# Optimization experiments

Measured on AMD Instinct MI355X. Metric: run time of the kernel, lower is better.

The kernel has to match this reference:

```python
import jax, jax.numpy as jnp
import numpy as np

N, B, S, A = 4, 32768, 512, 64
H = 256          # hidden_size
NH = 16          # effective number of heads = attend_dim (range(attend_dim) bug in source)
D = 16           # attend_dim = hidden // attend_heads
EPS_BN = 1e-5


def setup_inputs() -> dict:
    key = jax.random.key(0)
    ks = jax.random.split(key, 16)
    sc = 0.05
    return {
        "states": jax.random.normal(ks[0], (N, B, S), dtype=jnp.float32),
        "actions": jax.random.normal(ks[1], (N, B, A), dtype=jnp.float32),
        # per-agent state+action encoder (enc_fc1)
        "Wenc": jax.random.normal(ks[2], (N, S + A, H), dtype=jnp.float32) * sc,
        "benc": jax.random.normal(ks[3], (N, H), dtype=jnp.float32) * sc,
        # per-agent state encoder (s_enc_fc1)
        "Ws": jax.random.normal(ks[4], (N, S, H), dtype=jnp.float32) * sc,
        "bs": jax.random.normal(ks[5], (N, H), dtype=jnp.float32) * sc,
        # shared per-head extractors (no bias on key/selector; bias on value)
        "Wk": jax.random.normal(ks[6], (NH, H, D), dtype=jnp.float32) * sc,
        "Wsel": jax.random.normal(ks[7], (NH, H, D), dtype=jnp.float32) * sc,
        "Wv": jax.random.normal(ks[8], (NH, H, D), dtype=jnp.float32) * sc,
        "bv": jax.random.normal(ks[9], (NH, D), dtype=jnp.float32) * sc,
        # per-agent critic MLP (input = H + NH*D = 2H)
        "Wc1": jax.random.normal(ks[10], (N, 2 * H, H), dtype=jnp.float32) * sc,
        "bc1": jax.random.normal(ks[11], (N, H), dtype=jnp.float32) * sc,
        "Wc2": jax.random.normal(ks[12], (N, H, A), dtype=jnp.float32) * sc,
        "bc2": jax.random.normal(ks[13], (N, A), dtype=jnp.float32) * sc,
    }


def _lrelu(x):
    return jax.nn.leaky_relu(x, 0.01)


def _bn(x):
    # BatchNorm1d(affine=False), training mode: biased batch stats over batch axis
    m = x.mean(axis=1, keepdims=True)
    v = x.var(axis=1, keepdims=True)
    return (x - m) * jax.lax.rsqrt(v + EPS_BN)


def reference(states, actions, Wenc, benc, Ws, bs, Wk, Wsel, Wv, bv, Wc1, bc1, Wc2, bc2):
    n, b = states.shape[0], states.shape[1]
    # state+action encodings per agent: [n, B, H]
    sa = jnp.concatenate([states, actions], axis=-1)
    sa_enc = _lrelu(jnp.einsum('nbi,nih->nbh', _bn(sa), Wenc) + benc[:, None, :])
    # state encodings per agent: [n, B, H]
    s_enc = _lrelu(jnp.einsum('nbs,nsh->nbh', _bn(states), Ws) + bs[:, None, :])
    # per-head keys/values/selectors: [NH, n, B, D]
    keys = jnp.einsum('nbh,ehd->enbd', sa_enc, Wk)
    vals = _lrelu(jnp.einsum('nbh,ehd->enbd', sa_enc, Wv) + bv[:, None, None, :])
    sel = jnp.einsum('nbh,ehd->enbd', s_enc, Wsel)
    # attention of agent i over agents j != i (self excluded via -inf mask)
    logits = jnp.einsum('eibd,ejbd->eibj', sel, keys) / jnp.sqrt(jnp.float32(D))
    self_mask = jnp.eye(n, dtype=bool)[None, :, None, :]  # [1, i, 1, j]
    probs = jax.nn.softmax(jnp.where(self_mask, -1e9, logits), axis=-1)
    # weighted values: [n, B, NH, D] (head-major concat order)
    other = jnp.einsum('eibj,ejbd->ibed', probs, vals)
    critic_in = jnp.concatenate([s_enc, other.reshape(n, b, NH * D)], axis=-1)  # [n, B, 2H]
    h = _lrelu(jnp.einsum('nbc,nch->nbh', critic_in, Wc1) + bc1[:, None, :])
    all_q = jnp.einsum('nbh,nha->nba', h, Wc2) + bc2[:, None, :]  # [n, B, A]
    idx = jnp.argmax(actions, axis=-1)  # [n, B]
    q = jnp.take_along_axis(all_q, idx[..., None], axis=-1)  # [n, B, 1]
    return q
```

## Files before the change

kernel.cpp:

```cpp
#include <hip/hip_runtime.h>
#include <hip/hip_bf16.h>
#include <cstdint>
#include <cstddef>

using bf16 = __hip_bfloat16;
typedef __attribute__((ext_vector_type(8))) short bf16x8v;
typedef __attribute__((ext_vector_type(4))) short bf16x4v;
typedef __attribute__((ext_vector_type(4))) float f32x4v;

constexpr int Nn = 4;
constexpr int Bb = 32768;
constexpr int Ss = 512;
constexpr int Av = 64;
constexpr int SA = 576;
constexpr float BN_EPS = 1e-5f;

__device__ __forceinline__ float lrelu(float v){ return v >= 0.f ? v : 0.01f * v; }
__device__ __forceinline__ float bf2f(bf16 x){ return __bfloat162float(x); }
__device__ __forceinline__ short f2bf(float v){
  union { bf16 b; short s; } u; u.b = __float2bfloat16(v); return u.s;
}

__device__ __forceinline__ void gload16(const void* g, void* l){
  __builtin_amdgcn_global_load_lds(
      (const __attribute__((address_space(1))) unsigned int*)g,
      (__attribute__((address_space(3))) unsigned int*)l, 16, 0, 0);
}

template<bool WRX>
__global__ __launch_bounds__(256) void conv_stats(const float* __restrict__ states,
                                                  const float* __restrict__ actions,
                                                  float* __restrict__ ssum,
                                                  float* __restrict__ ssq,
                                                  short* __restrict__ Xbf){
  const int n  = blockIdx.z;
  const int tx = threadIdx.x;
  const int ty = threadIdx.y;
  const int g  = blockIdx.x * 64 + tx;
  const bool on = g < (SA / 4);
  const int f  = g * 4;
  const float* p = nullptr; int step = 0;
  if (on){
    if (f < Ss){ p = states  + (size_t)n*Bb*Ss + f;        step = Ss; }
    else       { p = actions + (size_t)n*Bb*Av + (f - Ss); step = Av; }
  }
  float s0=0.f,s1=0.f,s2=0.f,s3=0.f,q0=0.f,q1=0.f,q2=0.f,q3=0.f;
  const int b0 = blockIdx.y * 512 + ty, bend = blockIdx.y * 512 + 512;
  if (on){
    for (int b = b0; b < bend; b += 4){
      float4 v = *(const float4*)(p + (size_t)b*step);
      if (WRX){
        short t4[4] __attribute__((aligned(8))) =
            { f2bf(v.x), f2bf(v.y), f2bf(v.z), f2bf(v.w) };
        *(bf16x4v*)&Xbf[((size_t)n*Bb + b)*SA + f] = *(bf16x4v*)t4;
      }
      s0 += v.x; q0 += v.x*v.x;
      s1 += v.y; q1 += v.y*v.y;
      s2 += v.z; q2 += v.z*v.z;
      s3 += v.w; q3 += v.w*v.w;
    }
  }
  __shared__ float rs[4][64][4], rq[4][64][4];
  rs[ty][tx][0]=s0; rs[ty][tx][1]=s1; rs[ty][tx][2]=s2; rs[ty][tx][3]=s3;
  rq[ty][tx][0]=q0; rq[ty][tx][1]=q1; rq[ty][tx][2]=q2; rq[ty][tx][3]=q3;
  __syncthreads();
  if (ty == 0 && on){
    #pragma unroll
    for (int j = 0; j < 4; j++){
      float ts = rs[0][tx][j]+rs[1][tx][j]+rs[2][tx][j]+rs[3][tx][j];
      float tq = rq[0][tx][j]+rq[1][tx][j]+rq[2][tx][j]+rq[3][tx][j];
      atomicAdd(&ssum[n*SA + f + j], ts);
      atomicAdd(&ssq [n*SA + f + j], tq);
    }
  }
}

__global__ void bn_finalize(const float* __restrict__ ssum, const float* __restrict__ ssq,
                            float* __restrict__ mean, float* __restrict__ rstd){
  int i = blockIdx.x * 256 + threadIdx.x;
  float m = ssum[i] * (1.f / Bb);
  float v = ssq[i] * (1.f / Bb) - m * m;
  v = fmaxf(v, 0.f);
  mean[i] = m;
  rstd[i] = rsqrtf(v + BN_EPS);
}

__global__ void bias_copy(const float* __restrict__ benc, const float* __restrict__ bsx,
                          float* __restrict__ besc){
  int i = blockIdx.x * 256 + threadIdx.x;
  if (i < Nn*512){
    int a = i >> 9, c = i & 511;
    besc[i] = (c < 256) ? benc[a*256 + c] : bsx[a*256 + (c - 256)];
  }
}

template<int HEAD>
__global__ __launch_bounds__(256) void foldT2(const float* __restrict__ src,
                                              const float* __restrict__ scale,
                                              const float* __restrict__ mean,
                                              float* __restrict__ bias_out,
                                              short* __restrict__ dst,
                                              int Ks, int Kd, int N,
                                              int aDst, int biasStride){
  const int a  = blockIdx.z;
  const int tx = threadIdx.x & 63;
  const int ty = threadIdx.x >> 6;
  const int f0 = blockIdx.x * 64 + ty * 16;
  const int c  = blockIdx.y * 64 + tx;
  const float* s = src + (HEAD ? 0 : (size_t)a*Ks*N);
  short tmp[16] __attribute__((aligned(16)));
  float bsum = 0.f;
  #pragma unroll
  for (int j = 0; j < 16; j++){
    const int f = f0 + j;
    float w = 0.f;
    if (f < Ks){
      w = HEAD ? s[(((size_t)(c >> 4))*Ks + f)*16 + (c & 15)]
               : s[(size_t)f*N + c];
      if (scale) w *= scale[a*SA + f];
      if (mean)  bsum += mean[a*SA + f] * w;
    }
    tmp[j] = f2bf(w);
  }
  short* d = dst + (size_t)a*aDst + (size_t)c*Kd + f0;
  *(bf16x8v*)d       = *(bf16x8v*)tmp;
  *(bf16x8v*)(d + 8) = *(bf16x8v*)(tmp + 8);
  if (mean){
    __shared__ float red[4][64];
    red[ty][tx] = bsum;
    __syncthreads();
    if (threadIdx.x < 64){
      float t = red[0][threadIdx.x] + red[1][threadIdx.x]
              + red[2][threadIdx.x] + red[3][threadIdx.x];
      atomicAdd(&bias_out[a*biasStride + blockIdx.y*64 + threadIdx.x], -t);
    }
  }
}

template<int BM,int BN,int WM,int WN,int K,int ASRC,int AP,bool ACT,bool OUTF32,int MODE>
__global__ __launch_bounds__(256) void mgemm2(const void* A1, const void* A2,
                                              const short* __restrict__ Wp, int wPerAgent,
                                              const float* __restrict__ bias, int biasStride,
                                              void* Out, int outPitch){
  __shared__ __align__(16) short As[BM*32];
  __shared__ __align__(16) short Bs[BN*32];
  const int tid  = threadIdx.x;
  const int a    = blockIdx.z;
  const int row0 = blockIdx.x * BM;
  const int col0 = blockIdx.y * BN;
  const short* Wb = Wp + (size_t)a * wPerAgent;
  constexpr int FM = BM/WM/16, FN = BN/WN/16;
  const int wid = tid >> 6, lane = tid & 63;
  const int wm = wid % WM, wn = wid / WM;
  const int rowB = wm*(BM/WM), colB = wn*(BN/WN);
  const int lrow = lane & 15, lq = lane >> 4;
  const int srow = lane >> 2;
  const int skc  = ((lane & 3) ^ ((srow >> 1) & 3)) * 8;
  const int rq   = lq ^ ((lrow >> 1) & 3);

  f32x4v acc[FM][FN];
  #pragma unroll
  for (int i = 0; i < FM; i++)
    #pragma unroll
    for (int j = 0; j < FN; j++) acc[i][j] = (f32x4v){0.f,0.f,0.f,0.f};

  constexpr int AB = BM/16;
  constexpr int BB = BN/16;

  for (int k0 = 0; k0 < K; k0 += 32){
    #pragma unroll
    for (int t = 0; t < AB/4; t++){
      const int bb = wid + t*4;
      const int r  = bb*16 + srow;
      const int f  = k0 + skc;
      const short* src;
      if constexpr (ASRC == 3)
        src = (f < 256) ? (const short*)A1 + ((size_t)a*Bb + row0 + r)*(size_t)AP + f
                        : (const short*)A2 + ((size_t)a*Bb + row0 + r)*256 + (f - 256);
      else
        src = (const short*)A1 + ((size_t)a*Bb + row0 + r)*(size_t)AP + f;
      gload16(src, &As[bb*512]);
    }
    #pragma unroll
    for (int t = 0; t < BB/4; t++){
      const int bb = wid + t*4;
      const int r  = bb*16 + srow;
      const short* src = Wb + (size_t)(col0 + r)*K + k0 + skc;
      gload16(src, &Bs[bb*512]);
    }
    __syncthreads();
    bf16x8v af[FM], bfr[FN];
    #pragma unroll
    for (int mi = 0; mi < FM; mi++)
      af[mi] = *(const bf16x8v*)&As[(rowB + mi*16 + lrow)*32 + rq*8];
    #pragma unroll
    for (int ni = 0; ni < FN; ni++)
      bfr[ni] = *(const bf16x8v*)&Bs[(colB + ni*16 + lrow)*32 + rq*8];
    #pragma unroll
    for (int mi = 0; mi < FM; mi++)
      #pragma unroll
      for (int ni = 0; ni < FN; ni++)
        acc[mi][ni] = __builtin_amdgcn_mfma_f32_16x16x32_bf16(af[mi], bfr[ni], acc[mi][ni], 0, 0, 0);
    __syncthreads();
  }
  #pragma unroll
  for (int mi = 0; mi < FM; mi++){
    const size_t gr = (size_t)a*Bb + row0 + rowB + mi*16 + lq*4;
    #pragma unroll
    for (int ni = 0; ni < FN; ni++){
      const int gc = col0 + colB + ni*16 + lrow;
      float bb; bool doact;
      if constexpr (MODE == 1){
        doact = (gc >= 256);
        bb = doact ? bias[gc - 256] : 0.f;
      } else {
        bb = bias ? bias[a*biasStride + gc] : 0.f;
        doact = ACT;
      }
      #pragma unroll
      for (int r = 0; r < 4; r++){
        float v = acc[mi][ni][r] + bb;
        if (doact) v = lrelu(v);
        if constexpr (OUTF32) ((float*)Out)[(gr + r)*(size_t)outPitch + gc] = v;
        else                  ((bf16*) Out)[(gr + r)*(size_t)outPitch + gc] = __float2bfloat16(v);
      }
    }
  }
}

union B8g { uint4 u; bf16 h[8]; };
__global__ __launch_bounds__(256) void attn_g(const bf16* __restrict__ KV,
                                              bf16* SO){
  const int t = blockIdx.x * 256 + threadIdx.x;
  const int e = t & 15;
  const size_t b = t >> 4;
  const size_t ofsKV = b*512 + e*16;
  const size_t ofsS  = b*256 + e*16;
  float S[4][16], Kf[4][16], Vf[4][16];
  #pragma unroll
  for (int i = 0; i < 4; i++){
    B8g u0, u1;
    const bf16* sp = SO + (size_t)i*Bb*256 + ofsS;
    u0.u = *(const uint4*)sp; u1.u = *(const uint4*)(sp + 8);
    #pragma unroll
    for (int l = 0; l < 8; l++){ S[i][l] = bf2f(u0.h[l]); S[i][8+l] = bf2f(u1.h[l]); }
    const bf16* kp = KV + (size_t)i*Bb*512 + ofsKV;
    u0.u = *(const uint4*)kp; u1.u = *(const uint4*)(kp + 8);
    #pragma unroll
    for (int l = 0; l < 8; l++){ Kf[i][l] = bf2f(u0.h[l]); Kf[i][8+l] = bf2f(u1.h[l]); }
    const bf16* vp = kp + 256;
    u0.u = *(const uint4*)vp; u1.u = *(const uint4*)(vp + 8);
    #pragma unroll
    for (int l = 0; l < 8; l++){ Vf[i][l] = bf2f(u0.h[l]); Vf[i][8+l] = bf2f(u1.h[l]); }
  }
  #pragma unroll
  for (int i = 0; i < 4; i++){
    float lg[4];
    #pragma unroll
    for (int j = 0; j < 4; j++){
      float d = 0.f;
      #pragma unroll
      for (int l = 0; l < 16; l++) d += S[i][l] * Kf[j][l];
      lg[j] = d * 0.25f;
    }
    lg[i] = -1e9f;
    float m = fmaxf(fmaxf(lg[0], lg[1]), fmaxf(lg[2], lg[3]));
    float p[4], s = 0.f;
    #pragma unroll
    for (int j = 0; j < 4; j++){ p[j] = expf(lg[j] - m); s += p[j]; }
    p[i] = 0.f;
    const float inv = 1.f / s;
    float o[16] = {};
    #pragma unroll
    for (int j = 0; j < 4; j++){
      const float pj = p[j] * inv;
      #pragma unroll
      for (int l = 0; l < 16; l++) o[l] += pj * Vf[j][l];
    }
    B8g w0, w1;
    #pragma unroll
    for (int l = 0; l < 8; l++){ w0.h[l] = __float2bfloat16(o[l]); w1.h[l] = __float2bfloat16(o[8+l]); }
    bf16* op = SO + (size_t)i*Bb*256 + ofsS;
    *(uint4*)op       = w0.u;
    *(uint4*)(op + 8) = w1.u;
  }
}

__global__ __launch_bounds__(256) void sel_q(const float* __restrict__ actions,
                                             const float* __restrict__ allq,
                                             float* __restrict__ out){
  const size_t i = (size_t)blockIdx.x * 256 + threadIdx.x;
  const float* ap = actions + i*64;
  float best = ap[0]; int bi = 0;
  for (int j = 1; j < 64; j++){
    float v = ap[j];
    if (v > best){ best = v; bi = j; }
  }
  out[i] = allq[i*64 + bi];
}

constexpr int RB = 4;

template<int K>
__device__ __forceinline__ void gemm4_glb(const float* __restrict__ st,
                                          const float* __restrict__ ac,
                                          const float* __restrict__ mean,
                                          const float* __restrict__ rstd,
                                          int a, int brow0, int tid,
                                          const float* __restrict__ W,
                                          const float* __restrict__ bias, bool act,
                                          float (*Xs)[68], float (*Wt)[264],
                                          float (*Sout)[256]){
  const int r = tid >> 6, c4 = (tid & 63) * 4;
  float acc[4] = {};
  for (int k0 = 0; k0 < K; k0 += 8){
    if (tid < 32){
      const int rb = tid >> 3, kq = tid & 7;
      const int f = k0 + kq;
      float v = (f < Ss) ? st[((size_t)a*Bb + brow0 + rb)*Ss + f]
                         : ac[((size_t)a*Bb + brow0 + rb)*Av + (f - Ss)];
      Xs[kq][rb] = (v - mean[a*SA + f]) * rstd[a*SA + f];
    }
    {
      const int wk = tid >> 5, wc = (tid & 31) * 8;
      const float* wp = W + (size_t)(k0 + wk) * 256 + wc;
      *(float4*)&Wt[wk][wc]     = *(const float4*)wp;
      *(float4*)&Wt[wk][wc + 4] = *(const float4*)(wp + 4);
    }
    __syncthreads();
    #pragma unroll
    for (int kk = 0; kk < 8; kk++){
      const float av = Xs[kk][r];
      float4 w = *(const float4*)&Wt[kk][c4];
      acc[0] += av*w.x; acc[1] += av*w.y; acc[2] += av*w.z; acc[3] += av*w.w;
    }
    __syncthreads();
  }
  float4 o;
  o.x = acc[0] + (bias ? bias[c4+0] : 0.f);
  o.y = acc[1] + (bias ? bias[c4+1] : 0.f);
  o.z = acc[2] + (bias ? bias[c4+2] : 0.f);
  o.w = acc[3] + (bias ? bias[c4+3] : 0.f);
  if (act){ o.x = lrelu(o.x); o.y = lrelu(o.y); o.z = lrelu(o.z); o.w = lrelu(o.w); }
  *(float4*)&Sout[a*RB + r][c4] = o;
}

template<int K, bool HEAD>
__device__ __forceinline__ void gemm4_lds(const float (*S1)[256], const float (*S2)[256],
                                          int a, int tid,
                                          const float* __restrict__ W,
                                          const float* __restrict__ bias, bool act,
                                          float (*Wt)[264], float (*Sout)[256]){
  const int r = tid >> 6, c4 = (tid & 63) * 4;
  float acc[4] = {};
  for (int k0 = 0; k0 < K; k0 += 8){
    if (HEAD){
      const int wk = tid >> 5, c8 = (tid & 31) * 8;
      const int e = c8 >> 4, d0 = c8 & 15;
      const float* wp = W + (size_t)e*(256*16) + (size_t)(k0 + wk)*16 + d0;
      *(float4*)&Wt[wk][c8]     = *(const float4*)wp;
      *(float4*)&Wt[wk][c8 + 4] = *(const float4*)(wp + 4);
    } else {
      const int wk = tid >> 5, wc = (tid & 31) * 8;
      const float* wp = W + (size_t)(k0 + wk)*256 + wc;
      *(float4*)&Wt[wk][wc]     = *(const float4*)wp;
      *(float4*)&Wt[wk][wc + 4] = *(const float4*)(wp + 4);
    }
    __syncthreads();
    const float (*src)[256] = (k0 < 256) ? S1 : S2;
    const int kb = (k0 < 256) ? k0 : k0 - 256;
    const float* arow = &src[a*RB + r][kb];
    #pragma unroll
    for (int kk = 0; kk < 8; kk++){
      const float av = arow[kk];
      float4 w = *(const float4*)&Wt[kk][c4];
      acc[0] += av*w.x; acc[1] += av*w.y; acc[2] += av*w.z; acc[3] += av*w.w;
    }
    __syncthreads();
  }
  float4 o;
  o.x = acc[0] + (bias ? bias[c4+0] : 0.f);
  o.y = acc[1] + (bias ? bias[c4+1] : 0.f);
  o.z = acc[2] + (bias ? bias[c4+2] : 0.f);
  o.w = acc[3] + (bias ? bias[c4+3] : 0.f);
  if (act){ o.x = lrelu(o.x); o.y = lrelu(o.y); o.z = lrelu(o.z); o.w = lrelu(o.w); }
  *(float4*)&Sout[a*RB + r][c4] = o;
}

__global__ __launch_bounds__(256) void fused(
    const float* __restrict__ states, const float* __restrict__ actions,
    const float* __restrict__ mean,  const float* __restrict__ rstd,
    const float* __restrict__ Wenc, const float* __restrict__ benc,
    const float* __restrict__ Wsx,  const float* __restrict__ bsx,
    const float* __restrict__ Wk,   const float* __restrict__ Wsel,
    const float* __restrict__ Wv,   const float* __restrict__ bv,
    const float* __restrict__ Wc1,  const float* __restrict__ bc1,
    const float* __restrict__ Wc2,  const float* __restrict__ bc2,
    float* __restrict__ qout){
  __shared__ float A [16][256];
  __shared__ float Bs2[16][256];
  __shared__ float C [16][256];
  __shared__ float Wt[8][264];
  __shared__ float Xs[8][68];
  __shared__ float Cq[4][68];
  const int tid   = threadIdx.x;
  const int brow0 = blockIdx.x * RB;
  for (int a = 0; a < Nn; a++)
    gemm4_glb<Ss>(states, actions, mean, rstd, a, brow0, tid,
                  Wsx + (size_t)a*Ss*256, bsx + a*256, true, Xs, Wt, A);
  __syncthreads();
  for (int a = 0; a < Nn; a++)
    gemm4_lds<256, true>(A, nullptr, a, tid, Wsel, nullptr, false, Wt, C);
  __syncthreads();
  for (int a = 0; a < Nn; a++)
    gemm4_glb<SA>(states, actions, mean, rstd, a, brow0, tid,
                  Wenc + (size_t)a*SA*256, benc + a*256, true, Xs, Wt, A);
  __syncthreads();
  for (int a = 0; a < Nn; a++)
    gemm4_lds<256, true>(A, nullptr, a, tid, Wk, nullptr, false, Wt, Bs2);
  __syncthreads();
  for (int a = 0; a < Nn; a++)
    gemm4_lds<256, true>(A, nullptr, a, tid, Wv, bv, true, Wt, A);
  __syncthreads();
  if (tid < 64){
    const int rb = tid >> 4, e = tid & 15;
    const int co = e * 16;
    float S[4][16], Kf[4][16], Vf[4][16];
    #pragma unroll
    for (int i = 0; i < 4; i++)
      #pragma unroll
      for (int l = 0; l < 16; l++){
        S[i][l]  = C  [i*RB + rb][co + l];
        Kf[i][l] = Bs2[i*RB + rb][co + l];
        Vf[i][l] = A  [i*RB + rb][co + l];
      }
    #pragma unroll
    for (int i = 0; i < 4; i++){
      float lg[4];
      #pragma unroll
      for (int j = 0; j < 4; j++){
        float d = 0.f;
        #pragma unroll
        for (int l = 0; l < 16; l++) d += S[i][l] * Kf[j][l];
        lg[j] = d * 0.25f;
      }
      lg[i] = -1e9f;
      float m = fmaxf(fmaxf(lg[0], lg[1]), fmaxf(lg[2], lg[3]));
      float p[4], s = 0.f;
      #pragma unroll
      for (int j = 0; j < 4; j++){ p[j] = expf(lg[j] - m); s += p[j]; }
      p[i] = 0.f;
      const float inv = 1.f / s;
      float o[16] = {};
      #pragma unroll
      for (int j = 0; j < 4; j++){
        const float pj = p[j] * inv;
        #pragma unroll
        for (int l = 0; l < 16; l++) o[l] += pj * Vf[j][l];
      }
      #pragma unroll
      for (int l = 0; l < 16; l++) C[i*RB + rb][co + l] = o[l];
    }
  }
  __syncthreads();
  for (int a = 0; a < Nn; a++)
    gemm4_glb<Ss>(states, actions, mean, rstd, a, brow0, tid,
                  Wsx + (size_t)a*Ss*256, bsx + a*256, true, Xs, Wt, A);
  __syncthreads();
  for (int a = 0; a < Nn; a++)
    gemm4_lds<512, false>(A, C, a, tid, Wc1 + (size_t)a*512*256, bc1 + a*256, true, Wt, Bs2);
  __syncthreads();
  for (int a = 0; a < Nn; a++){
    const int r2 = tid >> 6, c2 = tid & 63;
    float acc = 0.f;
    for (int k0 = 0; k0 < 256; k0 += 8){
      const int wk = tid >> 5, wc = (tid & 31) * 2;
      const float* wp = Wc2 + (size_t)a*256*64 + (size_t)(k0 + wk)*64 + wc;
      Wt[wk][wc]     = wp[0];
      Wt[wk][wc + 1] = wp[1];
      __syncthreads();
      #pragma unroll
      for (int kk = 0; kk < 8; kk++) acc += Bs2[a*RB + r2][k0 + kk] * Wt[kk][c2];
      __syncthreads();
    }
    Cq[r2][c2] = acc + bc2[a*64 + c2];
    __syncthreads();
    if (tid < RB){
      const float* ap = actions + ((size_t)a*Bb + brow0 + tid)*Av;
      float best = ap[0]; int bi = 0;
      for (int j = 1; j < Av; j++){
        float v = ap[j];
        if (v > best){ best = v; bi = j; }
      }
      qout[(size_t)a*Bb + brow0 + tid] = Cq[tid][bi];
    }
    __syncthreads();
  }
}

extern "C" void kernel_launch(void* const* d_in, const int* in_sizes, int n_in,
                              void* d_out, int out_size, void* d_ws, size_t ws_size,
                              hipStream_t stream){
  (void)in_sizes; (void)n_in; (void)out_size;
  const float* states  = (const float*)d_in[0];
  const float* actions = (const float*)d_in[1];
  const float* Wenc    = (const float*)d_in[2];
  const float* benc    = (const float*)d_in[3];
  const float* Wsx     = (const float*)d_in[4];
  const float* bsx     = (const float*)d_in[5];
  const float* Wk      = (const float*)d_in[6];
  const float* Wsel    = (const float*)d_in[7];
  const float* Wv      = (const float*)d_in[8];
  const float* bv      = (const float*)d_in[9];
  const float* Wc1     = (const float*)d_in[10];
  const float* bc1     = (const float*)d_in[11];
  const float* Wc2     = (const float*)d_in[12];
  const float* bc2     = (const float*)d_in[13];
  float* qout = (float*)d_out;

  char* base = (char*)d_ws;
  float* ssum = (float*)base;
  float* ssq  = ssum + Nn*SA;
  float* mean = ssq  + Nn*SA;
  float* rstd = mean + Nn*SA;
  size_t off = 4*Nn*SA*sizeof(float);
  float* besc  = (float*)(base + off); off += Nn*512*sizeof(float);
  short* Wes_p = (short*)(base + off); off += (size_t)Nn*512*SA*2;
  short* Wkv_p = (short*)(base + off); off += 512*256*2;
  short* Whs_p = (short*)(base + off); off += 256*256*2;
  short* Wc1_p = (short*)(base + off); off += (size_t)Nn*256*512*2;
  short* Wc2_p = (short*)(base + off); off += (size_t)Nn*64*256*2;
  const size_t XBFB = (size_t)Nn*Bb*SA*2;
  const size_t W512 = (size_t)Nn*Bb*512*2;
  short* Xbf = (short*)(base + off);
  bf16*  SEL = (bf16*)(base + off);
  float* ALLQ= (float*)(base + off);
  off += XBFB;
  bf16* ES = (bf16*)(base + off); off += W512;
  bf16* KV = (bf16*)(base + off); off += W512;
  bf16* H  = KV;
  const size_t need = off;

  hipMemsetAsync(ssum, 0, 2*Nn*SA*sizeof(float), stream);

  if (ws_size >= need){
    conv_stats<true><<<dim3(3, 64, Nn), dim3(64, 4), 0, stream>>>(states, actions, ssum, ssq, Xbf);
    bn_finalize<<<dim3(9), dim3(256), 0, stream>>>(ssum, ssq, mean, rstd);

    bias_copy<<<dim3(8), 256, 0, stream>>>(benc, bsx, besc);
    foldT2<0><<<dim3(9, 4, Nn), 256, 0, stream>>>(Wenc, rstd, mean, besc,       Wes_p,            SA, SA, 256, 512*SA, 512);
    foldT2<0><<<dim3(9, 4, Nn), 256, 0, stream>>>(Wsx,  rstd, mean, besc + 256, Wes_p + 256*SA,   Ss, SA, 256, 512*SA, 512);
    foldT2<1><<<dim3(4, 4, 1), 256, 0, stream>>>(Wk,   nullptr, nullptr, nullptr, Wkv_p,           256, 256, 256, 0, 0);
    foldT2<1><<<dim3(4, 4, 1), 256, 0, stream>>>(Wv,   nullptr, nullptr, nullptr, Wkv_p + 256*256, 256, 256, 256, 0, 0);
    foldT2<1><<<dim3(4, 4, 1), 256, 0, stream>>>(Wsel, nullptr, nullptr, nullptr, Whs_p,           256, 256, 256, 0, 0);
    foldT2<0><<<dim3(8, 4, Nn), 256, 0, stream>>>(Wc1, nullptr, nullptr, nullptr, Wc1_p,           512, 512, 256, 256*512, 0);
    foldT2<0><<<dim3(4, 1, Nn), 256, 0, stream>>>(Wc2, nullptr, nullptr, nullptr, Wc2_p,           256, 256, 64,  64*256,  0);

    mgemm2<64,256,1,4,576,2,SA,true,false,0><<<dim3(Bb/64, 2, Nn), 256, 0, stream>>>(
        Xbf, nullptr, Wes_p, 512*SA, besc, 512, ES, 512);
    mgemm2<64,256,1,4,256,2,512,false,false,1><<<dim3(Bb/64, 2, Nn), 256, 0, stream>>>(
        ES, nullptr, Wkv_p, 0, bv, 0, KV, 512);
    mgemm2<64,256,1,4,256,2,512,false,false,0><<<dim3(Bb/64, 1, Nn), 256, 0, stream>>>(
        (const short*)ES + 256, nullptr, Whs_p, 0, nullptr, 0, SEL, 256);
    attn_g<<<dim3(Bb*16/256), 256, 0, stream>>>(KV, SEL);
    mgemm2<64,256,1,4,512,3,512,true,false,0><<<dim3(Bb/64, 1, Nn), 256, 0, stream>>>(
        (const short*)ES + 256, SEL, Wc1_p, 256*512, bc1, 256, H, 256);
    mgemm2<64,64,1,4,256,2,256,false,true,0><<<dim3(Bb/64, 1, Nn), 256, 0, stream>>>(
        H, nullptr, Wc2_p, 64*256, bc2, 64, ALLQ, 64);
    sel_q<<<dim3(Nn*Bb/256), 256, 0, stream>>>(actions, ALLQ, qout);
  } else {
    conv_stats<false><<<dim3(3, 64, Nn), dim3(64, 4), 0, stream>>>(states, actions, ssum, ssq, nullptr);
    bn_finalize<<<dim3(9), dim3(256), 0, stream>>>(ssum, ssq, mean, rstd);
    fused<<<dim3(Bb/RB), 256, 0, stream>>>(states, actions, mean, rstd,
                                           Wenc, benc, Wsx, bsx,
                                           Wk, Wsel, Wv, bv,
                                           Wc1, bc1, Wc2, bc2, qout);
  }
}
```

Measured before the change: 909.5 us.

## Fuse argmax Q selection into final GEMM epilogue and retile GEMMs to 128x128

Adds a MODE 2 epilogue to the final critic GEMM. It stages the 64x64 Q tile in shared memory, computes the argmax over actions with a 4-lane shuffle reduction, and writes only the selected Q value. This removes the separate sel_q kernel and the fp32 ALLQ round trip through global memory. The other GEMMs also change tile shape from 64x256 (1x4 warps) to 128x128 (2x2 warps), which changes data reuse and grid size. The GEMM epilogue now reads the actions row from global memory, and argmax ties resolve to the lowest index.

After: 866.4 us. 1.05x faster.

```diff
diff --git a/kernel.cpp b/kernel.cpp
--- a/kernel.cpp
+++ b/kernel.cpp
@@ -203,26 +203,57 @@
         acc[mi][ni] = __builtin_amdgcn_mfma_f32_16x16x32_bf16(af[mi], bfr[ni], acc[mi][ni], 0, 0, 0);
     __syncthreads();
   }
-  #pragma unroll
-  for (int mi = 0; mi < FM; mi++){
-    const size_t gr = (size_t)a*Bb + row0 + rowB + mi*16 + lq*4;
-    #pragma unroll
-    for (int ni = 0; ni < FN; ni++){
-      const int gc = col0 + colB + ni*16 + lrow;
-      float bb; bool doact;
-      if constexpr (MODE == 1){
-        doact = (gc >= 256);
-        bb = doact ? bias[gc - 256] : 0.f;
-      } else {
-        bb = bias ? bias[a*biasStride + gc] : 0.f;
-        doact = ACT;
-      }
-      #pragma unroll
-      for (int r = 0; r < 4; r++){
-        float v = acc[mi][ni][r] + bb;
-        if (doact) v = lrelu(v);
-        if constexpr (OUTF32) ((float*)Out)[(gr + r)*(size_t)outPitch + gc] = v;
-        else                  ((bf16*) Out)[(gr + r)*(size_t)outPitch + gc] = __float2bfloat16(v);
+  if constexpr (MODE == 2){
+    __shared__ float Q[64][65];
+    #pragma unroll
+    for (int mi = 0; mi < FM; mi++){
+      const int qr = rowB + mi*16 + lq*4;
+      const int gc = colB + lrow;
+      const float bb = bias[a*biasStride + col0 + gc];
+      #pragma unroll
+      for (int r = 0; r < 4; r++)
+        Q[qr + r][gc] = acc[mi][0][r] + bb;
+    }
+    __syncthreads();
+    const int row = tid >> 2, seg = (tid & 3) * 16;
+    const float* ap = (const float*)A2 + ((size_t)a*Bb + row0 + row)*64 + seg;
+    float best = ap[0]; int bi = 0;
+    #pragma unroll
+    for (int j = 1; j < 16; j++){
+      float v = ap[j];
+      if (v > best){ best = v; bi = j; }
+    }
+    bi += seg;
+    #pragma unroll
+    for (int d = 1; d < 4; d <<= 1){
+      float ov = __shfl_xor(best, d);
+      int   oi = __shfl_xor(bi, d);
+      if (ov > best || (ov == best && oi < bi)){ best = ov; bi = oi; }
+    }
+    if ((tid & 3) == 0)
+      ((float*)Out)[(size_t)a*Bb + row0 + row] = Q[row][bi];
+  } else {
+    #pragma unroll
+    for (int mi = 0; mi < FM; mi++){
+      const size_t gr = (size_t)a*Bb + row0 + rowB + mi*16 + lq*4;
+      #pragma unroll
+      for (int ni = 0; ni < FN; ni++){
+        const int gc = col0 + colB + ni*16 + lrow;
+        float bb; bool doact;
+        if constexpr (MODE == 1){
+          doact = (gc >= 256);
+          bb = doact ? bias[gc - 256] : 0.f;
+        } else {
+          bb = bias ? bias[a*biasStride + gc] : 0.f;
+          doact = ACT;
+        }
+        #pragma unroll
+        for (int r = 0; r < 4; r++){
+          float v = acc[mi][ni][r] + bb;
+          if (doact) v = lrelu(v);
+          if constexpr (OUTF32) ((float*)Out)[(gr + r)*(size_t)outPitch + gc] = v;
+          else                  ((bf16*) Out)[(gr + r)*(size_t)outPitch + gc] = __float2bfloat16(v);
+        }
       }
     }
   }
@@ -284,19 +315,6 @@
     *(uint4*)op       = w0.u;
     *(uint4*)(op + 8) = w1.u;
   }
-}
-
-__global__ __launch_bounds__(256) void sel_q(const float* __restrict__ actions,
-                                             const float* __restrict__ allq,
-                                             float* __restrict__ out){
-  const size_t i = (size_t)blockIdx.x * 256 + threadIdx.x;
-  const float* ap = actions + i*64;
-  float best = ap[0]; int bi = 0;
-  for (int j = 1; j < 64; j++){
-    float v = ap[j];
-    if (v > best){ best = v; bi = j; }
-  }
-  out[i] = allq[i*64 + bi];
 }
 
 constexpr int RB = 4;
@@ -534,7 +552,6 @@
   const size_t W512 = (size_t)Nn*Bb*512*2;
   short* Xbf = (short*)(base + off);
   bf16*  SEL = (bf16*)(base + off);
-  float* ALLQ= (float*)(base + off);
   off += XBFB;
   bf16* ES = (bf16*)(base + off); off += W512;
   bf16* KV = (bf16*)(base + off); off += W512;
@@ -556,18 +573,17 @@
     foldT2<0><<<dim3(8, 4, Nn), 256, 0, stream>>>(Wc1, nullptr, nullptr, nullptr, Wc1_p,           512, 512, 256, 256*512, 0);
     foldT2<0><<<dim3(4, 1, Nn), 256, 0, stream>>>(Wc2, nullptr, nullptr, nullptr, Wc2_p,           256, 256, 64,  64*256,  0);
 
-    mgemm2<64,256,1,4,576,2,SA,true,false,0><<<dim3(Bb/64, 2, Nn), 256, 0, stream>>>(
+    mgemm2<128,128,2,2,576,2,SA,true,false,0><<<dim3(Bb/128, 4, Nn), 256, 0, stream>>>(
         Xbf, nullptr, Wes_p, 512*SA, besc, 512, ES, 512);
-    mgemm2<64,256,1,4,256,2,512,false,false,1><<<dim3(Bb/64, 2, Nn), 256, 0, stream>>>(
+    mgemm2<128,128,2,2,256,2,512,false,false,1><<<dim3(Bb/128, 4, Nn), 256, 0, stream>>>(
         ES, nullptr, Wkv_p, 0, bv, 0, KV, 512);
-    mgemm2<64,256,1,4,256,2,512,false,false,0><<<dim3(Bb/64, 1, Nn), 256, 0, stream>>>(
+    mgemm2<128,128,2,2,256,2,512,false,false,0><<<dim3(Bb/128, 2, Nn), 256, 0, stream>>>(
         (const short*)ES + 256, nullptr, Whs_p, 0, nullptr, 0, SEL, 256);
     attn_g<<<dim3(Bb*16/256), 256, 0, stream>>>(KV, SEL);
-    mgemm2<64,256,1,4,512,3,512,true,false,0><<<dim3(Bb/64, 1, Nn), 256, 0, stream>>>(
+    mgemm2<128,128,2,2,512,3,512,true,false,0><<<dim3(Bb/128, 2, Nn), 256, 0, stream>>>(
         (const short*)ES + 256, SEL, Wc1_p, 256*512, bc1, 256, H, 256);
-    mgemm2<64,64,1,4,256,2,256,false,true,0><<<dim3(Bb/64, 1, Nn), 256, 0, stream>>>(
-        H, nullptr, Wc2_p, 64*256, bc2, 64, ALLQ, 64);
-    sel_q<<<dim3(Nn*Bb/256), 256, 0, stream>>>(actions, ALLQ, qout);
+    mgemm2<64,64,1,4,256,2,256,false,false,2><<<dim3(Bb/64, 1, Nn), 256, 0, stream>>>(
+        H, actions, Wc2_p, 64*256, bc2, 64, qout, 0);
   } else {
     conv_stats<false><<<dim3(3, 64, Nn), dim3(64, 4), 0, stream>>>(states, actions, ssum, ssq, nullptr);
     bn_finalize<<<dim3(9), dim3(256), 0, stream>>>(ssum, ssq, mean, rstd);
```
